# Kernel optimization log

Hardware: AMD Instinct MI355X
Metric: run time of the kernel (lower is better)

Reference implementation:

```python
import jax, jax.numpy as jnp
from jax import lax
import numpy as np

H = 161  # input_size == hidden_size per the torch module


def _lstm(x, w_ih, w_hh, b_ih, b_hh, reverse):
    """Single-direction LSTM matching torch.nn.LSTM gate order (i, f, g, o).
    x: [B, T, I] -> returns hidden states [B, T, H]."""
    # Precompute the input contribution for all timesteps in one GEMM.
    pre = jnp.einsum('bti,gi->btg', x, w_ih) + b_ih + b_hh  # [B, T, 4H]
    B = x.shape[0]

    def step(carry, p):
        h, c = carry
        gates = p + h @ w_hh.T  # [B, 4H]
        i, f, g, o = jnp.split(gates, 4, axis=-1)
        c = jax.nn.sigmoid(f) * c + jax.nn.sigmoid(i) * jnp.tanh(g)
        h = jax.nn.sigmoid(o) * jnp.tanh(c)
        return (h, c), h

    init = (jnp.zeros((B, H), x.dtype), jnp.zeros((B, H), x.dtype))
    _, hs = lax.scan(step, init, jnp.swapaxes(pre, 0, 1), reverse=reverse)
    return jnp.swapaxes(hs, 0, 1)  # [B, T, H]


def _block(h, p, relu):
    # p = (wih_f, whh_f, bih_f, bhh_f, wih_b, whh_b, bih_b, bhh_b, W, b)
    f = _lstm(h, p[0], p[1], p[2], p[3], reverse=False)
    b = _lstm(h, p[4], p[5], p[6], p[7], reverse=True)
    out = jnp.concatenate([f, b], axis=-1) @ p[8].T + p[9]  # Linear(2H -> H)
    if relu:
        out = jax.nn.relu(out)
    return out + h  # residual


def _forward(x, p1, p2, p3):
    h = _block(x, p1, relu=True)
    h = _block(h, p2, relu=True)
    h = _block(h, p3, relu=False)  # block 3: no ReLU before residual in the torch code
    return h


def setup_inputs() -> dict:
    key = jax.random.key(0)
    ks = iter(jax.random.split(key, 64))
    s = 1.0 / np.sqrt(H)  # torch LSTM/Linear default uniform init scale

    def u(shape):
        return jax.random.uniform(next(ks), shape, jnp.float32, -s, s)

    inp = {"x": jax.random.normal(next(ks), (32, 1000, H), jnp.float32)}
    shapes = [("wih_f", (4 * H, H)), ("whh_f", (4 * H, H)), ("bih_f", (4 * H,)), ("bhh_f", (4 * H,)),
              ("wih_b", (4 * H, H)), ("whh_b", (4 * H, H)), ("bih_b", (4 * H,)), ("bhh_b", (4 * H,)),
              ("W", (H, 2 * H)), ("bl", (H,))]
    for i in (1, 2, 3):
        for nm, sh in shapes:
            inp[f"l{i}_{nm}"] = u(sh)
    return inp


def reference(x,
              l1_wih_f, l1_whh_f, l1_bih_f, l1_bhh_f, l1_wih_b, l1_whh_b, l1_bih_b, l1_bhh_b, l1_W, l1_bl,
              l2_wih_f, l2_whh_f, l2_bih_f, l2_bhh_f, l2_wih_b, l2_whh_b, l2_bih_b, l2_bhh_b, l2_W, l2_bl,
              l3_wih_f, l3_whh_f, l3_bih_f, l3_bhh_f, l3_wih_b, l3_whh_b, l3_bih_b, l3_bhh_b, l3_W, l3_bl):
    p1 = (l1_wih_f, l1_whh_f, l1_bih_f, l1_bhh_f, l1_wih_b, l1_whh_b, l1_bih_b, l1_bhh_b, l1_W, l1_bl)
    p2 = (l2_wih_f, l2_whh_f, l2_bih_f, l2_bhh_f, l2_wih_b, l2_whh_b, l2_bih_b, l2_bhh_b, l2_W, l2_bl)
    p3 = (l3_wih_f, l3_whh_f, l3_bih_f, l3_bhh_f, l3_wih_b, l3_whh_b, l3_bih_b, l3_bhh_b, l3_W, l3_bl)
    return _forward(x, p1, p2, p3)
```

## Files before the change

### kernel.cpp

```cpp
#include <hip/hip_runtime.h>
#include <hip/hip_fp16.h>

#define H 161
#define G4 644
#define BB 32
#define TT 1000
#define M_TOT (BB*TT)
#define KXP 192
#define KLP 352
#define NWIH 1344
#define NPAIR 84
#define NVEC (NPAIR/4)

typedef _Float16 h2_t  __attribute__((ext_vector_type(2)));
typedef _Float16 f16x8 __attribute__((ext_vector_type(8)));
typedef float    f32x4 __attribute__((ext_vector_type(4)));

__device__ __forceinline__ h2_t bc_h2(unsigned int u) {
    return __builtin_bit_cast(h2_t, u);
}

__device__ __forceinline__ float dot2f(h2_t a, h2_t b, float c) {
#if __has_builtin(__builtin_amdgcn_fdot2)
    return __builtin_amdgcn_fdot2(a, b, c, false);
#else
    return c + (float)a[0] * (float)b[0] + (float)a[1] * (float)b[1];
#endif
}

__device__ __forceinline__ float tanh_f(float x) {
    return 1.0f - 2.0f / (__expf(2.0f * x) + 1.0f);
}

template<int CTRL>
__device__ __forceinline__ float dpp_qp(float x) {
    int y = __builtin_amdgcn_update_dpp(0, __builtin_bit_cast(int, x),
                                        CTRL, 0xF, 0xF, true);
    return __builtin_bit_cast(float, y);
}

__device__ __forceinline__ void bar_lds() {
    __builtin_amdgcn_sched_barrier(0);
    asm volatile("s_waitcnt lgkmcnt(0)" ::: "memory");
    __builtin_amdgcn_s_barrier();
    __builtin_amdgcn_sched_barrier(0);
}

__global__ __launch_bounds__(256) void cvt_x(
    const float* __restrict__ in,
    __half* __restrict__ out)
{
    const int total = M_TOT * KXP;
    for (int idx = blockIdx.x * 256 + threadIdx.x; idx < total;
         idx += gridDim.x * 256) {
        int m = idx / KXP, k = idx - m * KXP;
        float v = (k < H) ? in[(size_t)m * H + k] : (k == H ? 1.f : 0.f);
        out[idx] = __float2half(v);
    }
}

__global__ __launch_bounds__(256) void cvt_wih3(
    const float* __restrict__ wf0, const float* __restrict__ wb0,
    const float* __restrict__ bif0, const float* __restrict__ bhf0,
    const float* __restrict__ bib0, const float* __restrict__ bhb0,
    const float* __restrict__ wf1, const float* __restrict__ wb1,
    const float* __restrict__ bif1, const float* __restrict__ bhf1,
    const float* __restrict__ bib1, const float* __restrict__ bhb1,
    const float* __restrict__ wf2, const float* __restrict__ wb2,
    const float* __restrict__ bif2, const float* __restrict__ bhf2,
    const float* __restrict__ bib2, const float* __restrict__ bhb2,
    __half* __restrict__ out)
{
    const int l = blockIdx.y;
    const float* wf  = (l == 0) ? wf0  : (l == 1) ? wf1  : wf2;
    const float* wb  = (l == 0) ? wb0  : (l == 1) ? wb1  : wb2;
    const float* bif = (l == 0) ? bif0 : (l == 1) ? bif1 : bif2;
    const float* bhf = (l == 0) ? bhf0 : (l == 1) ? bhf1 : bhf2;
    const float* bib = (l == 0) ? bib0 : (l == 1) ? bib1 : bib2;
    const float* bhb = (l == 0) ? bhb0 : (l == 1) ? bhb1 : bhb2;
    __half* o = out + (size_t)l * NWIH * KXP;

    const int total = NWIH * KXP;
    for (int idx = blockIdx.x * 256 + threadIdx.x; idx < total;
         idx += gridDim.x * 256) {
        int n = idx / KXP, k = idx - n * KXP;
        float v = 0.f;
        if (n < G4) {
            v = (k < H) ? wf[(size_t)n * H + k]
                        : (k == H ? bif[n] + bhf[n] : 0.f);
        } else if (n < 2 * G4) {
            int g = n - G4;
            v = (k < H) ? wb[(size_t)g * H + k]
                        : (k == H ? bib[g] + bhb[g] : 0.f);
        }
        o[idx] = __float2half(v);
    }
}

__global__ __launch_bounds__(256) void cvt_W3(
    const float* __restrict__ W0, const float* __restrict__ W1,
    const float* __restrict__ W2,
    __half* __restrict__ out)
{
    const int l = blockIdx.y;
    const float* W = (l == 0) ? W0 : (l == 1) ? W1 : W2;
    __half* o = out + (size_t)l * 192 * KLP;

    const int total = 192 * KLP;
    for (int idx = blockIdx.x * 256 + threadIdx.x; idx < total;
         idx += gridDim.x * 256) {
        int n = idx / KLP, k = idx - n * KLP;
        float v = (n < H && k < 2 * H) ? W[(size_t)n * (2 * H) + k] : 0.f;
        o[idx] = __float2half(v);
    }
}

__global__ __launch_bounds__(256) void pre_mfma(
    const __half* __restrict__ A16,
    const __half* __restrict__ Wih16,
    __half* __restrict__ pre)
{
    const int m0 = blockIdx.x * 64;
    const int n0b = blockIdx.y * 192;
    const int tid = threadIdx.x;
    const int wv = tid >> 6, l = tid & 63;
    const int wm = wv & 1, wn = wv >> 1;
    const int cl = l & 15, kg = l >> 4;

    const __half* ap = A16 + (size_t)(m0 + wm * 32 + cl) * KXP + kg * 8;
    f16x8 xa0[6], xa1[6];
    #pragma unroll
    for (int kt = 0; kt < 6; ++kt) {
        xa0[kt] = *(const f16x8*)(ap + kt * 32);
        xa1[kt] = *(const f16x8*)(ap + 16 * KXP + kt * 32);
    }

    for (int nb = 0; nb < 3; ++nb) {
        const int n0 = n0b + nb * 64;
        const __half* wp = Wih16 + (size_t)(n0 + wn * 32 + cl) * KXP + kg * 8;

        f32x4 acc[2][2] = {};
        #pragma unroll
        for (int kt = 0; kt < 6; ++kt) {
            f16x8 w0 = *(const f16x8*)(wp + kt * 32);
            f16x8 w1 = *(const f16x8*)(wp + 16 * KXP + kt * 32);
            acc[0][0] = __builtin_amdgcn_mfma_f32_16x16x32_f16(w0, xa0[kt], acc[0][0], 0, 0, 0);
            acc[0][1] = __builtin_amdgcn_mfma_f32_16x16x32_f16(w0, xa1[kt], acc[0][1], 0, 0, 0);
            acc[1][0] = __builtin_amdgcn_mfma_f32_16x16x32_f16(w1, xa0[kt], acc[1][0], 0, 0, 0);
            acc[1][1] = __builtin_amdgcn_mfma_f32_16x16x32_f16(w1, xa1[kt], acc[1][1], 0, 0, 0);
        }

        #pragma unroll
        for (int sn = 0; sn < 2; ++sn)
            #pragma unroll
            for (int sm = 0; sm < 2; ++sm) {
                int n = n0 + wn * 32 + sn * 16 + kg * 4;
                int m = m0 + wm * 32 + sm * 16 + cl;
                if (n < 2 * G4) {
                    int d = (n >= G4) ? 1 : 0;
                    int g = n - d * G4;
                    __half2 lo, hi;
                    lo.x = __float2half(acc[sn][sm][0]);
                    lo.y = __float2half(acc[sn][sm][1]);
                    hi.x = __float2half(acc[sn][sm][2]);
                    hi.y = __float2half(acc[sn][sm][3]);
                    __half* dst = pre + ((size_t)d * M_TOT + m) * G4 + g;
                    *(__half2*)dst = lo;
                    *(__half2*)(dst + 2) = hi;
                }
            }
    }
}

__global__ __launch_bounds__(256) void lin_mfma(
    const __half* __restrict__ Hc,
    const __half* __restrict__ W16,
    const float* __restrict__ bl,
    const float* __restrict__ res,
    float* __restrict__ out,
    __half* __restrict__ A16out,
    int relu, int wr_a16)
{
    const int m0 = blockIdx.x * 64, n0 = blockIdx.y * 64;
    const int tid = threadIdx.x;
    const int wv = tid >> 6, l = tid & 63;
    const int wm = wv & 1, wn = wv >> 1;
    const int cl = l & 15, kg = l >> 4;

    const __half* ap = Hc  + (size_t)(m0 + wm * 32 + cl) * KLP + kg * 8;
    const __half* wp = W16 + (size_t)(n0 + wn * 32 + cl) * KLP + kg * 8;

    f32x4 acc[2][2] = {};
    #pragma unroll
    for (int kt = 0; kt < 11; ++kt) {
        f16x8 w0 = *(const f16x8*)(wp + kt * 32);
        f16x8 w1 = *(const f16x8*)(wp + 16 * KLP + kt * 32);
        f16x8 x0 = *(const f16x8*)(ap + kt * 32);
        f16x8 x1 = *(const f16x8*)(ap + 16 * KLP + kt * 32);
        acc[0][0] = __builtin_amdgcn_mfma_f32_16x16x32_f16(w0, x0, acc[0][0], 0, 0, 0);
        acc[0][1] = __builtin_amdgcn_mfma_f32_16x16x32_f16(w0, x1, acc[0][1], 0, 0, 0);
        acc[1][0] = __builtin_amdgcn_mfma_f32_16x16x32_f16(w1, x0, acc[1][0], 0, 0, 0);
        acc[1][1] = __builtin_amdgcn_mfma_f32_16x16x32_f16(w1, x1, acc[1][1], 0, 0, 0);
    }

    #pragma unroll
    for (int sn = 0; sn < 2; ++sn)
        #pragma unroll
        for (int sm = 0; sm < 2; ++sm) {
            int nb = n0 + wn * 32 + sn * 16 + kg * 4;
            int m  = m0 + wm * 32 + sm * 16 + cl;
            #pragma unroll
            for (int r = 0; r < 4; ++r) {
                int n = nb + r;
                if (n < H) {
                    float v = acc[sn][sm][r] + bl[n];
                    if (relu) v = fmaxf(v, 0.f);
                    v += res[(size_t)m * H + n];
                    out[(size_t)m * H + n] = v;
                    if (wr_a16)
                        A16out[(size_t)m * KXP + n] = __float2half(v);
                }
            }
        }
}

__global__ __launch_bounds__(704, 3) void lstm_scan(
    const __half* __restrict__ pre,
    const float* __restrict__ whh_f,
    const float* __restrict__ whh_b,
    __half* __restrict__ hcat)
{
    const int b = blockIdx.x;
    const int d = blockIdx.y;
    const int tid = threadIdx.x;
    const int l = tid & 63, wv = tid >> 6;
    const int gate = l & 3;
    const int hid = wv * 16 + (l >> 2);
    const int hidc = (hid < H) ? hid : (H - 1);
    const bool writer = (gate == 0) && (hid < H);
    const bool is_g = (gate == 2);
    const float* whh = d ? whh_b : whh_f;

    __shared__ __align__(16) unsigned int h_sh[2][NPAIR];

    h2_t w[NPAIR];
    {
        const float* row = whh + (size_t)(gate * H + hidc) * H;
        #pragma unroll
        for (int i = 0; i < NPAIR; ++i) {
            float w0 = (2 * i < H) ? row[2 * i] : 0.f;
            float w1 = (2 * i + 1 < H) ? row[2 * i + 1] : 0.f;
            h2_t v; v[0] = (_Float16)w0; v[1] = (_Float16)w1;
            w[i] = v;
        }
    }
    if (tid < 2 * NPAIR) ((unsigned int*)h_sh)[tid] = 0u;

    float c = 0.f;
    const __half* pb = pre + ((size_t)d * M_TOT + (size_t)b * TT) * G4
                           + gate * H + hidc;

    #define LDP(tt_) ({ int tc_ = ((tt_) < TT) ? (tt_) : (TT - 1);          \
                        int t_  = d ? (TT - 1 - tc_) : tc_;                 \
                        pb[(size_t)t_ * G4]; })

    __half p0 = LDP(0), p1 = LDP(1);
    __syncthreads();

    #define STEP(TTT, PJ, BUF) {                                            \
        int t = d ? (TT - 1 - (TTT)) : (TTT);                               \
        float pc = __half2float(PJ);                                        \
        PJ = LDP((TTT) + 2);                    \
        float a0 = 0.f, a1 = 0.f, a2 = 0.f, a3 = 0.f;                       \
        const uint4* hv = (const uint4*)h_sh[BUF];                          \
        _Pragma("unroll")                                                   \
        for (int i = 0; i < NVEC; ++i) {                                    \
            uint4 hh = hv[i];                                               \
            a0 = dot2f(w[4 * i + 0], bc_h2(hh.x), a0);                      \
            a1 = dot2f(w[4 * i + 1], bc_h2(hh.y), a1);                      \
            a2 = dot2f(w[4 * i + 2], bc_h2(hh.z), a2);                      \
            a3 = dot2f(w[4 * i + 3], bc_h2(hh.w), a3);                      \
        }                                                                   \
        float acc = pc + (a0 + a1) + (a2 + a3);                             \
        float xs = is_g ? (acc + acc) : acc;                                \
        float s = 1.0f / (1.0f + __expf(-xs));                              \
        float act = is_g ? (s + s - 1.0f) : s;                              \
        float fA = dpp_qp<0xB1>(act);           \
        float gA = dpp_qp<0x4E>(act);           \
        float oA = dpp_qp<0x1B>(act);           \
        c = fA * c + act * gA;               \
        float hval = oA * tanh_f(c);                                        \
        if (writer) {                                                       \
            __half h16 = __float2half(hval);                                \
            hcat[((size_t)b * TT + t) * KLP + (size_t)d * H + hid] = h16;   \
            ((__half*)h_sh[(BUF) ^ 1])[hid] = h16;                          \
        }                                                                   \
        bar_lds();                                                          \
    }

    for (int base = 0; base < TT; base += 2) {
        STEP(base,     p0, 0)
        STEP(base + 1, p1, 1)
    }
    #undef STEP
    #undef LDP
}

extern "C" void kernel_launch(void* const* d_in, const int* in_sizes, int n_in,
                              void* d_out, int out_size, void* d_ws, size_t ws_size,
                              hipStream_t stream) {
    const float* x = (const float*)d_in[0];

    char* ws = (char*)d_ws;
    __half* pre    = (__half*)ws;
    __half* hcat16 = (__half*)(ws + (size_t)2 * M_TOT * G4 * 2);
    __half* A16    = (__half*)((char*)hcat16 + (size_t)M_TOT * KLP * 2);
    __half* wih3   = (__half*)((char*)A16 + (size_t)M_TOT * KXP * 2);
    __half* W3     = (__half*)((char*)wih3 + (size_t)3 * NWIH * KXP * 2);
    float*  bufA   = (float*)((char*)W3 + (size_t)3 * 192 * KLP * 2);
    float*  bufB   = bufA + (size_t)M_TOT * H;

    const float* const* p0 = (const float* const*)(d_in + 1);
    const float* const* p1 = (const float* const*)(d_in + 11);
    const float* const* p2 = (const float* const*)(d_in + 21);

    hipMemsetAsync(hcat16, 0, (size_t)M_TOT * KLP * sizeof(__half), stream);
    cvt_x<<<2048, 256, 0, stream>>>(x, A16);
    cvt_wih3<<<dim3(256, 3), 256, 0, stream>>>(
        p0[0], p0[4], p0[2], p0[3], p0[6], p0[7],
        p1[0], p1[4], p1[2], p1[3], p1[6], p1[7],
        p2[0], p2[4], p2[2], p2[3], p2[6], p2[7], wih3);
    cvt_W3<<<dim3(64, 3), 256, 0, stream>>>(p0[8], p1[8], p2[8], W3);

    const float* const* ps[3] = {p0, p1, p2};
    const float* cur = x;
    float* outs[3] = {bufA, bufB, (float*)d_out};

    for (int l = 0; l < 3; ++l) {
        const float* const* p = ps[l];
        pre_mfma<<<dim3(M_TOT / 64, 7), 256, 0, stream>>>(
            A16, wih3 + (size_t)l * NWIH * KXP, pre);
        lstm_scan<<<dim3(32, 2), 704, 0, stream>>>(pre, p[1], p[5], hcat16);
        lin_mfma<<<dim3(M_TOT / 64, 3), 256, 0, stream>>>(
            hcat16, W3 + (size_t)l * 192 * KLP, p[9], cur, outs[l], A16,
            (l < 2) ? 1 : 0, (l < 2) ? 1 : 0);
        cur = outs[l];
    }
}
```

Measured before the change: 3.507 ms.

## Split LSTM recurrence K-dimension across quad lanes with DPP reduction

Each quad of lanes now owns one hidden unit and splits the recurrent dot product over the K dimension. Each lane computes partial sums for all four gates over a quarter of h, and a DPP butterfly reduces them across the quad. Each lane therefore reads a quarter of the h vector from LDS instead of all of it, cutting LDS traffic per step, at the cost of extra cross-lane reduction ops. Register usage for weights stays at 84 words, and h is stored in a padded 4x48 layout.

```diff
diff --git a/kernel.cpp b/kernel.cpp
--- a/kernel.cpp
+++ b/kernel.cpp
@@ -9,8 +9,9 @@
 #define KXP 192
 #define KLP 352
 #define NWIH 1344
-#define NPAIR 84
-#define NVEC (NPAIR/4)
+#define QD 42
+#define QH 48
+#define QP 21
 
 typedef _Float16 h2_t  __attribute__((ext_vector_type(2)));
 typedef _Float16 f16x8 __attribute__((ext_vector_type(8)));
@@ -38,6 +39,17 @@
                                         CTRL, 0xF, 0xF, true);
     return __builtin_bit_cast(float, y);
 }
+template<int CTRL>
+__device__ __forceinline__ float dpp_addf(float x) {
+    int y = __builtin_amdgcn_update_dpp(0, __builtin_bit_cast(int, x),
+                                        CTRL, 0xF, 0xF, true);
+    return x + __builtin_bit_cast(float, y);
+}
+__device__ __forceinline__ float qsum(float x) {
+    x = dpp_addf<0xB1>(x);
+    x = dpp_addf<0x4E>(x);
+    return x;
+}
 
 __device__ __forceinline__ void bar_lds() {
     __builtin_amdgcn_sched_barrier(0);
@@ -47,8 +59,7 @@
 }
 
 __global__ __launch_bounds__(256) void cvt_x(
-    const float* __restrict__ in,
-    __half* __restrict__ out)
+    const float* __restrict__ in, __half* __restrict__ out)
 {
     const int total = M_TOT * KXP;
     for (int idx = blockIdx.x * 256 + threadIdx.x; idx < total;
@@ -233,32 +244,35 @@
     const int b = blockIdx.x;
     const int d = blockIdx.y;
     const int tid = threadIdx.x;
-    const int l = tid & 63, wv = tid >> 6;
-    const int gate = l & 3;
-    const int hid = wv * 16 + (l >> 2);
-    const int hidc = (hid < H) ? hid : (H - 1);
-    const bool writer = (gate == 0) && (hid < H);
-    const bool is_g = (gate == 2);
+    const int s = tid & 3;
+    const int q = tid >> 2;
+    const int qc = (q < H) ? q : (H - 1);
+    const bool writer = (s == 0) && (q < H);
+    const bool is_g = (s == 2);
     const float* whh = d ? whh_b : whh_f;
 
-    __shared__ __align__(16) unsigned int h_sh[2][NPAIR];
-
-    h2_t w[NPAIR];
-    {
-        const float* row = whh + (size_t)(gate * H + hidc) * H;
+    __shared__ __align__(16) __half h_sh[2][4][QH];
+
+    unsigned int w[4][QP];
+    #pragma unroll
+    for (int g = 0; g < 4; ++g) {
+        const float* row = whh + (size_t)(g * H + qc) * H;
         #pragma unroll
-        for (int i = 0; i < NPAIR; ++i) {
-            float w0 = (2 * i < H) ? row[2 * i] : 0.f;
-            float w1 = (2 * i + 1 < H) ? row[2 * i + 1] : 0.f;
+        for (int j = 0; j < QP; ++j) {
+            int k = s * QD + 2 * j;
+            float w0 = (k < H) ? row[k] : 0.f;
+            float w1 = (k + 1 < H) ? row[k + 1] : 0.f;
             h2_t v; v[0] = (_Float16)w0; v[1] = (_Float16)w1;
-            w[i] = v;
+            w[g][j] = __builtin_bit_cast(unsigned int, v);
         }
     }
-    if (tid < 2 * NPAIR) ((unsigned int*)h_sh)[tid] = 0u;
+    if (tid < 2 * 4 * QH / 2) ((unsigned int*)h_sh)[tid] = 0u;
+
+    const int wqq = qc / QD, wqi = qc - wqq * QD;
 
     float c = 0.f;
     const __half* pb = pre + ((size_t)d * M_TOT + (size_t)b * TT) * G4
-                           + gate * H + hidc;
+                           + s * H + qc;
 
     #define LDP(tt_) ({ int tc_ = ((tt_) < TT) ? (tt_) : (TT - 1);          \
                         int t_  = d ? (TT - 1 - tc_) : tc_;                 \
@@ -271,29 +285,59 @@
         int t = d ? (TT - 1 - (TTT)) : (TTT);                               \
         float pc = __half2float(PJ);                                        \
         PJ = LDP((TTT) + 2);                    \
-        float a0 = 0.f, a1 = 0.f, a2 = 0.f, a3 = 0.f;                       \
-        const uint4* hv = (const uint4*)h_sh[BUF];                          \
+                             \
+        float ai = (s == 0) ? pc : 0.f;                                     \
+        float af = (s == 1) ? pc : 0.f;                                     \
+        float ag = (s == 2) ? pc : 0.f;                                     \
+        float ao = (s == 3) ? pc : 0.f;                                     \
+        const __half* hq = h_sh[BUF][s];                                    \
+        const uint4* h4 = (const uint4*)hq;                                 \
         _Pragma("unroll")                                                   \
-        for (int i = 0; i < NVEC; ++i) {                                    \
-            uint4 hh = hv[i];                                               \
-            a0 = dot2f(w[4 * i + 0], bc_h2(hh.x), a0);                      \
-            a1 = dot2f(w[4 * i + 1], bc_h2(hh.y), a1);                      \
-            a2 = dot2f(w[4 * i + 2], bc_h2(hh.z), a2);                      \
-            a3 = dot2f(w[4 * i + 3], bc_h2(hh.w), a3);                      \
+        for (int j = 0; j < 5; ++j) {                                       \
+            uint4 hh = h4[j];                                               \
+            h2_t hx = bc_h2(hh.x), hy = bc_h2(hh.y);                        \
+            h2_t hz = bc_h2(hh.z), hw = bc_h2(hh.w);                        \
+            ai = dot2f(bc_h2(w[0][4*j+0]), hx, ai);                         \
+            ai = dot2f(bc_h2(w[0][4*j+1]), hy, ai);                         \
+            ai = dot2f(bc_h2(w[0][4*j+2]), hz, ai);                         \
+            ai = dot2f(bc_h2(w[0][4*j+3]), hw, ai);                         \
+            af = dot2f(bc_h2(w[1][4*j+0]), hx, af);                         \
+            af = dot2f(bc_h2(w[1][4*j+1]), hy, af);                         \
+            af = dot2f(bc_h2(w[1][4*j+2]), hz, af);                         \
+            af = dot2f(bc_h2(w[1][4*j+3]), hw, af);                         \
+            ag = dot2f(bc_h2(w[2][4*j+0]), hx, ag);                         \
+            ag = dot2f(bc_h2(w[2][4*j+1]), hy, ag);                         \
+            ag = dot2f(bc_h2(w[2][4*j+2]), hz, ag);                         \
+            ag = dot2f(bc_h2(w[2][4*j+3]), hw, ag);                         \
+            ao = dot2f(bc_h2(w[3][4*j+0]), hx, ao);                         \
+            ao = dot2f(bc_h2(w[3][4*j+1]), hy, ao);                         \
+            ao = dot2f(bc_h2(w[3][4*j+2]), hz, ao);                         \
+            ao = dot2f(bc_h2(w[3][4*j+3]), hw, ao);                         \
         }                                                                   \
-        float acc = pc + (a0 + a1) + (a2 + a3);                             \
-        float xs = is_g ? (acc + acc) : acc;                                \
-        float s = 1.0f / (1.0f + __expf(-xs));                              \
-        float act = is_g ? (s + s - 1.0f) : s;                              \
-        float fA = dpp_qp<0xB1>(act);           \
-        float gA = dpp_qp<0x4E>(act);           \
-        float oA = dpp_qp<0x1B>(act);           \
-        c = fA * c + act * gA;               \
+        {                       \
+            h2_t hl = bc_h2(((const unsigned int*)hq)[20]);                 \
+            ai = dot2f(bc_h2(w[0][20]), hl, ai);                            \
+            af = dot2f(bc_h2(w[1][20]), hl, af);                            \
+            ag = dot2f(bc_h2(w[2][20]), hl, ag);                            \
+            ao = dot2f(bc_h2(w[3][20]), hl, ao);                            \
+        }                                                                   \
+                 \
+        ai = qsum(ai); af = qsum(af); ag = qsum(ag); ao = qsum(ao);         \
+                                       \
+        float own = (s == 0) ? ai : (s == 1) ? af : (s == 2) ? ag : ao;     \
+        float xs = is_g ? (own + own) : own;                                \
+        float sg = 1.0f / (1.0f + __expf(-xs));                             \
+        float act = is_g ? (sg + sg - 1.0f) : sg;                           \
+                    \
+        float fA = dpp_qp<0xB1>(act);                                       \
+        float gA = dpp_qp<0x4E>(act);                                       \
+        float oA = dpp_qp<0x1B>(act);                                       \
+        c = fA * c + act * gA;                                              \
         float hval = oA * tanh_f(c);                                        \
         if (writer) {                                                       \
             __half h16 = __float2half(hval);                                \
-            hcat[((size_t)b * TT + t) * KLP + (size_t)d * H + hid] = h16;   \
-            ((__half*)h_sh[(BUF) ^ 1])[hid] = h16;                          \
+            hcat[((size_t)b * TT + t) * KLP + (size_t)d * H + q] = h16;     \
+            h_sh[(BUF) ^ 1][wqq][wqi] = h16;                                \
         }                                                                   \
         bar_lds();                                                          \
     }
```

After: 3.292 ms. 6.2% less time.
